# Optimization experiments

Hardware: AMD Instinct MI355X
Metric: run time of the kernel (lower is better)

## Reference

```python
import jax, jax.numpy as jnp
import numpy as np

V, E, DIN, DH = 8192, 4096, 512, 256
N_CLASSES = 2
EPS = 1e-5  # torch LayerNorm default
EDGE_P = 0.004  # ~33 nodes per hyperedge


def layernorm(x, g, b):
    m = jnp.mean(x, axis=-1, keepdims=True)
    v = jnp.mean((x - m) ** 2, axis=-1, keepdims=True)
    return (x - m) / jnp.sqrt(v + EPS) * g + b


def setup_inputs() -> dict:
    key = jax.random.key(0)
    ks = jax.random.split(key, 8)
    X = jax.random.normal(ks[0], (V, DIN), dtype=jnp.float32)
    # binary incidence matrix (|V|, |E|)
    H_inc = (jax.random.uniform(ks[1], (V, E)) < EDGE_P).astype(jnp.float32)
    Wp = jax.random.normal(ks[2], (DH, DIN), dtype=jnp.float32) * 0.02  # input_proj (no bias)
    W0 = jax.random.normal(ks[3], (DH, DH), dtype=jnp.float32) * 0.02
    W1 = jax.random.normal(ks[4], (DH, DH), dtype=jnp.float32) * 0.02
    g0 = jnp.ones((DH,), jnp.float32); b0 = jnp.zeros((DH,), jnp.float32)
    g1 = jnp.ones((DH,), jnp.float32); b1 = jnp.zeros((DH,), jnp.float32)
    Wc = jax.random.normal(ks[5], (N_CLASSES, DH), dtype=jnp.float32) * 0.02
    bc = jnp.zeros((N_CLASSES,), jnp.float32)
    return {"X": X, "H_inc": H_inc, "Wp": Wp, "W0": W0, "W1": W1,
            "g0": g0, "b0": b0, "g1": g1, "b1": b1, "Wc": Wc, "bc": bc}


def reference(X, H_inc, Wp, W0, W1, g0, b0, g1, b1, Wc, bc):
    # --- normalized incidence: H_tilde = D_v^{-1/2} H D_e^{-1/2}, 0 for isolated ---
    d_v = H_inc.sum(axis=1)   # (V,)
    d_e = H_inc.sum(axis=0)   # (E,)
    dvi = jnp.where(d_v > 0, jnp.where(d_v > 0, d_v, 1.0) ** -0.5, 0.0)
    dei = jnp.where(d_e > 0, jnp.where(d_e > 0, d_e, 1.0) ** -0.5, 0.0)
    H_tilde = dvi[:, None] * H_inc * dei[None, :]            # (V, E)
    HHt = H_tilde @ H_tilde.T                                # (V, V)

    # input projection
    Xh = X @ Wp.T                                            # (V, DH)

    # L=2 message-passing layers with residual + LayerNorm
    for W, g, b in ((W0, g0, b0), (W1, g1, b1)):
        Xn = jax.nn.relu((HHt @ Xh) @ W.T)
        Xh = layernorm(Xh + Xn, g, b)

    # mean pool per hyperedge (== Python loop over E in the original):
    # z_e = mean of member node embeddings; zeros for empty hyperedges
    cnt = jnp.where(d_e > 0, d_e, 1.0)[:, None]              # (E, 1)
    z_E = (H_inc.T @ Xh) / cnt                               # (E, DH)

    logits = z_E @ Wc.T + bc                                 # (E, 2)
    return jax.nn.softmax(logits, axis=1)
```

## Files before the change

kernel.cpp:

```cpp
#include <hip/hip_runtime.h>
#include <math.h>

#define NV 8192
#define NE 4096
#define DIN 512
#define DH 256
#define CAP_E 96
#define CAP_V 64
#define NPROJ (NV / 32)
#define NSCAN (NV / 2)

#define OFF_XH   0
#define OFF_UB   (OFF_XH + NV*DH)
#define OFF_YB   (OFF_UB + NV*DH/2)
#define OFF_NCNT (OFF_YB + NE*DH/2)
#define OFF_ECNT (OFF_NCNT + NV)
#define OFF_EL   (OFF_ECNT + NE*16)
#define OFF_NL   (OFF_EL + NE*CAP_E)
#define OFF_XHB  (OFF_NL + NV*CAP_V)
#define OFF_Q    (OFF_XHB + NV*DH/2)

using bf16x8 = __attribute__((ext_vector_type(8))) short;
using f32x4  = __attribute__((ext_vector_type(4))) float;
using f32x4v = __attribute__((ext_vector_type(4))) float;

__device__ inline unsigned short f2bf(float f) {
    union { float f; unsigned u; } v; v.f = f;
    unsigned r = v.u + 0x7FFF + ((v.u >> 16) & 1);
    return (unsigned short)(r >> 16);
}
__device__ inline float b2f(unsigned short s) {
    union { unsigned u; float f; } v; v.u = ((unsigned)s) << 16; return v.f;
}

__device__ inline void u_gemm_from_lds(const short* __restrict__ sm,
                                       const float* __restrict__ W,
                                       unsigned short* __restrict__ Ub,
                                       int bm, int tid) {
    const int w = tid >> 6, lane = tid & 63;
    const int r15 = lane & 15, k8 = (lane >> 4) << 3;
    const int swz = lane ^ ((lane >> 3) & 6);
    f32x4 acc[2][4];
#pragma unroll
    for (int mi = 0; mi < 2; ++mi)
#pragma unroll
        for (int ni = 0; ni < 4; ++ni) acc[mi][ni] = (f32x4){0.f, 0.f, 0.f, 0.f};
#pragma unroll
    for (int kc = 0; kc < 8; ++kc) {
        bf16x8 af[2], bfr[4];
        af[0] = *(const bf16x8*)&sm[(0 * 8 + kc) * 512 + swz * 8];
        af[1] = *(const bf16x8*)&sm[(1 * 8 + kc) * 512 + swz * 8];
#pragma unroll
        for (int ni = 0; ni < 4; ++ni) {
            const float* wr = W + (size_t)(w * 64 + ni * 16 + r15) * DH + kc * 32 + k8;
            float4 b0 = *(const float4*)wr;
            float4 b1 = *(const float4*)(wr + 4);
            bf16x8 bv;
            bv[0] = (short)f2bf(b0.x); bv[1] = (short)f2bf(b0.y);
            bv[2] = (short)f2bf(b0.z); bv[3] = (short)f2bf(b0.w);
            bv[4] = (short)f2bf(b1.x); bv[5] = (short)f2bf(b1.y);
            bv[6] = (short)f2bf(b1.z); bv[7] = (short)f2bf(b1.w);
            bfr[ni] = bv;
        }
#pragma unroll
        for (int mi = 0; mi < 2; ++mi)
#pragma unroll
            for (int ni = 0; ni < 4; ++ni)
                acc[mi][ni] = __builtin_amdgcn_mfma_f32_16x16x32_bf16(
                    af[mi], bfr[ni], acc[mi][ni], 0, 0, 0);
    }
    const int quad = lane >> 4, cl = lane & 15;
#pragma unroll
    for (int mi = 0; mi < 2; ++mi)
#pragma unroll
        for (int ni = 0; ni < 4; ++ni)
#pragma unroll
            for (int r = 0; r < 4; ++r)
                Ub[(size_t)(bm + mi * 16 + quad * 4 + r) * DH + w * 64 + ni * 16 + cl]
                    = f2bf(acc[mi][ni][r]);
}

__global__ __launch_bounds__(256) void scan_proj(const float* __restrict__ H,
                                                 const float* __restrict__ X,
                                                 const float* __restrict__ Wp,
                                                 const float* __restrict__ W0,
                                                 float* __restrict__ Xh,
                                                 unsigned short* __restrict__ Ub,
                                                 int* __restrict__ edge_cnt,
                                                 int* __restrict__ node_cnt,
                                                 int* __restrict__ edge_list,
                                                 int* __restrict__ node_list) {
    __shared__ short AsBs[1024 + 8192];
    const int tid = threadIdx.x;
    if (blockIdx.x >= NPROJ) {
        const int w = tid >> 6, lane = tid & 63;
        const int v    = (blockIdx.x - NPROJ) * 2 + (w >> 1);
        const int half = w & 1;
        const f32x4v* H4 = (const f32x4v*)(H + (size_t)v * NE) + half * 512;
        f32x4v h[8];
#pragma unroll
        for (int it = 0; it < 8; ++it)
            h[it] = __builtin_nontemporal_load(&H4[lane + 64 * it]);
        unsigned m = 0u;
#pragma unroll
        for (int it = 0; it < 8; ++it) {
#pragma unroll
            for (int c = 0; c < 4; ++c)
                m |= (h[it][c] != 0.0f ? 1u : 0u) << (it * 4 + c);
        }
        int n = __builtin_popcount(m);
        int pre = n;
#pragma unroll
        for (int o = 1; o < 64; o <<= 1) {
            int t = __shfl_up(pre, o, 64);
            if (lane >= o) pre += t;
        }
        int total = __shfl(pre, 63, 64);
        int local = pre - n;
        int base = 0;
        if (lane == 0 && total > 0) base = atomicAdd(&node_cnt[v], total);
        base = __shfl(base, 0, 64) + local;
        const int ebase = half * 2048 + 4 * lane;
        int e_arr[4] = {0, 0, 0, 0};
        {
            unsigned mm = m;
#pragma unroll
            for (int u = 0; u < 4; ++u) {
                if (mm) {
                    int j = __builtin_ctz(mm);
                    mm &= mm - 1;
                    e_arr[u] = ebase + 256 * (j >> 2) + (j & 3);
                }
            }
        }
        int s_arr[4];
#pragma unroll
        for (int u = 0; u < 4; ++u)
            s_arr[u] = (u < n) ? atomicAdd(&edge_cnt[e_arr[u] << 4], 1) : 0;
#pragma unroll
        for (int u = 0; u < 4; ++u) {
            if (u < n) {
                if (s_arr[u] < CAP_E) edge_list[e_arr[u] * CAP_E + s_arr[u]] = v;
                int idx = base + u;
                if (idx < CAP_V) node_list[v * CAP_V + idx] = e_arr[u];
            }
        }
        if (n > 4) {
            unsigned mm = m;
            mm &= mm - 1; mm &= mm - 1; mm &= mm - 1; mm &= mm - 1;
            int k = 4;
            while (mm) {
                int j = __builtin_ctz(mm); mm &= mm - 1;
                int ee = ebase + 256 * (j >> 2) + (j & 3);
                int gc = atomicAdd(&edge_cnt[ee << 4], 1);
                if (gc < CAP_E) edge_list[ee * CAP_E + gc] = v;
                int idx = base + k;
                if (idx < CAP_V) node_list[v * CAP_V + idx] = ee;
                ++k;
            }
        }
        return;
    }
    short* As = AsBs;
    short* Bs = AsBs + 1024;
    const int K = DIN;
    const int lane = tid & 63;
    const int w    = tid >> 6;
    const int bm   = blockIdx.x * 32;
    const int swz  = lane ^ ((lane >> 3) & 6);
    float4 ar, br[8];
    ar = *(const float4*)(X + (size_t)(bm + (tid >> 3)) * K + ((tid & 7) << 2));
#pragma unroll
    for (int it = 0; it < 8; ++it) {
        int i = tid + it * 256;
        br[it] = *(const float4*)(Wp + (size_t)(i >> 3) * K + ((i & 7) << 2));
    }
    f32x4 acc[2][4];
#pragma unroll
    for (int mi = 0; mi < 2; ++mi)
#pragma unroll
        for (int ni = 0; ni < 4; ++ni) acc[mi][ni] = (f32x4){0.f, 0.f, 0.f, 0.f};
    for (int k0 = 0; k0 < K; k0 += 32) {
        __syncthreads();
        {
            int row = tid >> 3, kk = (tid & 7) << 2;
            int quad = kk >> 3, j = kk & 7;
            int ln = (row & 15) + (quad << 4);
            int pp = ln ^ ((ln >> 3) & 6);
            ushort4 u = {f2bf(ar.x), f2bf(ar.y), f2bf(ar.z), f2bf(ar.w)};
            *(ushort4*)&As[(row >> 4) * 512 + pp * 8 + j] = u;
        }
#pragma unroll
        for (int it = 0; it < 8; ++it) {
            int i = tid + it * 256;
            int row = i >> 3, kk = (i & 7) << 2;
            int quad = kk >> 3, j = kk & 7;
            int ln = (row & 15) + (quad << 4);
            int pp = ln ^ ((ln >> 3) & 6);
            float4 v = br[it];
            ushort4 u = {f2bf(v.x), f2bf(v.y), f2bf(v.z), f2bf(v.w)};
            *(ushort4*)&Bs[(row >> 4) * 512 + pp * 8 + j] = u;
        }
        __syncthreads();
        if (k0 + 32 < K) {
            int kn = k0 + 32;
            ar = *(const float4*)(X + (size_t)(bm + (tid >> 3)) * K + kn + ((tid & 7) << 2));
#pragma unroll
            for (int it = 0; it < 8; ++it) {
                int i = tid + it * 256;
                br[it] = *(const float4*)(Wp + (size_t)(i >> 3) * K + kn + ((i & 7) << 2));
            }
        }
        bf16x8 af[2], bfr[4];
        af[0] = *(const bf16x8*)&As[0 * 512 + swz * 8];
        af[1] = *(const bf16x8*)&As[1 * 512 + swz * 8];
#pragma unroll
        for (int ni = 0; ni < 4; ++ni)
            bfr[ni] = *(const bf16x8*)&Bs[(w * 4 + ni) * 512 + swz * 8];
#pragma unroll
        for (int mi = 0; mi < 2; ++mi)
#pragma unroll
            for (int ni = 0; ni < 4; ++ni)
                acc[mi][ni] = __builtin_amdgcn_mfma_f32_16x16x32_bf16(
                    af[mi], bfr[ni], acc[mi][ni], 0, 0, 0);
    }
    const int quad = lane >> 4, cl = lane & 15;
    __syncthreads();
#pragma unroll
    for (int mi = 0; mi < 2; ++mi)
#pragma unroll
        for (int ni = 0; ni < 4; ++ni)
#pragma unroll
            for (int r = 0; r < 4; ++r) {
                float v = acc[mi][ni][r];
                int rl  = mi * 16 + quad * 4 + r;
                int col = w * 64 + ni * 16 + cl;
                Xh[(size_t)(bm + rl) * DH + col] = v;
                int kc = col >> 5, kk = col & 31;
                int q2 = kk >> 3, j = kk & 7;
                int ln = (rl & 15) + (q2 << 4);
                int pp = ln ^ ((ln >> 3) & 6);
                AsBs[(mi * 8 + kc) * 512 + pp * 8 + j] = (short)f2bf(v);
            }
    __syncthreads();
    u_gemm_from_lds(AsBs, W0, Ub, bm, tid);
}

__global__ __launch_bounds__(256) void gemm_u(const unsigned short* __restrict__ A,
                                              const float* __restrict__ W,
                                              unsigned short* __restrict__ U) {
    const int K = DH;
    __shared__ short As[2048];
    __shared__ short Bs[16384];
    const int tid  = threadIdx.x;
    const int lane = tid & 63;
    const int w    = tid >> 6;
    const int bm   = blockIdx.x * 32;
    const int swz  = lane ^ ((lane >> 3) & 6);

    uint4 ar; float4 br[16];
    ar = *(const uint4*)(A + (size_t)(bm + (tid >> 3)) * K + ((tid & 7) << 3));
#pragma unroll
    for (int it = 0; it < 16; ++it) {
        int i = tid + it * 256;
        br[it] = *(const float4*)(W + (size_t)(i >> 4) * K + ((i & 15) << 2));
    }
    f32x4 acc[2][4];
#pragma unroll
    for (int mi = 0; mi < 2; ++mi)
#pragma unroll
        for (int ni = 0; ni < 4; ++ni) acc[mi][ni] = (f32x4){0.f, 0.f, 0.f, 0.f};

    for (int k0 = 0; k0 < K; k0 += 64) {
        __syncthreads();
        {
            int row = tid >> 3, kq = tid & 7;
            int kc = kq >> 2, quad = kq & 3;
            int ln = (row & 15) + (quad << 4);
            int pp = ln ^ ((ln >> 3) & 6);
            *(uint4*)&As[((row >> 4) * 2 + kc) * 512 + pp * 8] = ar;
        }
#pragma unroll
        for (int it = 0; it < 16; ++it) {
            int i = tid + it * 256;
            int row = i >> 4, kk = (i & 15) << 2;
            int kc = kk >> 5, quad = (kk >> 3) & 3, j = kk & 7;
            int ln = (row & 15) + (quad << 4);
            int pp = ln ^ ((ln >> 3) & 6);
            float4 v = br[it];
            ushort4 u = {f2bf(v.x), f2bf(v.y), f2bf(v.z), f2bf(v.w)};
            *(ushort4*)&Bs[((row >> 4) * 2 + kc) * 512 + pp * 8 + j] = u;
        }
        __syncthreads();
        if (k0 + 64 < K) {
            int kn = k0 + 64;
            ar = *(const uint4*)(A + (size_t)(bm + (tid >> 3)) * K + kn + ((tid & 7) << 3));
#pragma unroll
            for (int it = 0; it < 16; ++it) {
                int i = tid + it * 256;
                br[it] = *(const float4*)(W + (size_t)(i >> 4) * K + kn + ((i & 15) << 2));
            }
        }
#pragma unroll
        for (int kc = 0; kc < 2; ++kc) {
            bf16x8 af[2], bfr[4];
            af[0] = *(const bf16x8*)&As[(0 * 2 + kc) * 512 + swz * 8];
            af[1] = *(const bf16x8*)&As[(1 * 2 + kc) * 512 + swz * 8];
#pragma unroll
            for (int ni = 0; ni < 4; ++ni)
                bfr[ni] = *(const bf16x8*)&Bs[((w * 4 + ni) * 2 + kc) * 512 + swz * 8];
#pragma unroll
            for (int mi = 0; mi < 2; ++mi)
#pragma unroll
                for (int ni = 0; ni < 4; ++ni)
                    acc[mi][ni] = __builtin_amdgcn_mfma_f32_16x16x32_bf16(
                        af[mi], bfr[ni], acc[mi][ni], 0, 0, 0);
        }
    }
    const int quad = lane >> 4, cl = lane & 15;
#pragma unroll
    for (int mi = 0; mi < 2; ++mi)
#pragma unroll
        for (int ni = 0; ni < 4; ++ni)
#pragma unroll
            for (int r = 0; r < 4; ++r)
                U[(size_t)(bm + mi * 16 + quad * 4 + r) * DH + w * 64 + ni * 16 + cl]
                    = f2bf(acc[mi][ni][r]);
}

__global__ __launch_bounds__(64) void edge_gather(const unsigned short* __restrict__ Ub,
                                                  const int* __restrict__ edge_cnt,
                                                  const int* __restrict__ edge_list,
                                                  const int* __restrict__ node_cnt,
                                                  unsigned short* __restrict__ Yb) {
    int e = blockIdx.x;
    int tid = threadIdx.x;
    __shared__ int   lv[CAP_E];
    __shared__ float lc[CAP_E];
    int tc = edge_cnt[e << 4];
    int cnt = min(tc, CAP_E);
    for (int j = tid; j < cnt; j += 64) {
        int v = edge_list[e * CAP_E + j];
        lv[j] = v * (DH / 4);
        lc[j] = rsqrtf((float)node_cnt[v]);
    }
    __syncthreads();
    const ushort4* X4 = (const ushort4*)Ub;
    float4 a[8];
#pragma unroll
    for (int u = 0; u < 8; ++u) a[u] = (float4){0.f, 0.f, 0.f, 0.f};
    int i = 0;
    for (; i + 8 <= cnt; i += 8) {
#pragma unroll
        for (int u = 0; u < 8; ++u) {
            ushort4 h = X4[lv[i + u] + tid]; float c = lc[i + u];
            a[u].x = fmaf(c, b2f(h.x), a[u].x); a[u].y = fmaf(c, b2f(h.y), a[u].y);
            a[u].z = fmaf(c, b2f(h.z), a[u].z); a[u].w = fmaf(c, b2f(h.w), a[u].w);
        }
    }
    for (; i < cnt; ++i) {
        ushort4 h = X4[lv[i] + tid]; float c = lc[i];
        a[0].x = fmaf(c, b2f(h.x), a[0].x); a[0].y = fmaf(c, b2f(h.y), a[0].y);
        a[0].z = fmaf(c, b2f(h.z), a[0].z); a[0].w = fmaf(c, b2f(h.w), a[0].w);
    }
#pragma unroll
    for (int u = 4; u > 0; u >>= 1)
#pragma unroll
        for (int q = 0; q < u; ++q) {
            a[q].x += a[q + u].x; a[q].y += a[q + u].y;
            a[q].z += a[q + u].z; a[q].w += a[q + u].w;
        }
    float de = tc > 0 ? rsqrtf((float)tc) : 0.f;
    ushort4 o = {f2bf(de * a[0].x), f2bf(de * a[0].y),
                 f2bf(de * a[0].z), f2bf(de * a[0].w)};
    ((ushort4*)Yb)[e * (DH / 4) + tid] = o;
}

__global__ __launch_bounds__(64) void node_ln(const unsigned short* __restrict__ Yb,
                                              const int* __restrict__ node_cnt,
                                              const int* __restrict__ node_list,
                                              const int* __restrict__ edge_cnt,
                                              float* __restrict__ Xh,
                                              unsigned short* __restrict__ Xhb,
                                              const float* __restrict__ g,
                                              const float* __restrict__ b) {
    int v = blockIdx.x;
    int tid = threadIdx.x;
    __shared__ int   le[CAP_V];
    __shared__ float lc[CAP_V];
    int tc = node_cnt[v];
    int cnt = min(tc, CAP_V);
    if (tid < cnt) {
        int e = node_list[v * CAP_V + tid];
        le[tid] = e * (DH / 4);
        lc[tid] = rsqrtf((float)edge_cnt[e << 4]);
    }
    __syncthreads();
    const ushort4* Y4 = (const ushort4*)Yb;
    float4 a[8];
#pragma unroll
    for (int u = 0; u < 8; ++u) a[u] = (float4){0.f, 0.f, 0.f, 0.f};
    int i = 0;
    for (; i + 8 <= cnt; i += 8) {
#pragma unroll
        for (int u = 0; u < 8; ++u) {
            ushort4 h = Y4[le[i + u] + tid]; float c = lc[i + u];
            a[u].x = fmaf(c, b2f(h.x), a[u].x); a[u].y = fmaf(c, b2f(h.y), a[u].y);
            a[u].z = fmaf(c, b2f(h.z), a[u].z); a[u].w = fmaf(c, b2f(h.w), a[u].w);
        }
    }
    for (; i < cnt; ++i) {
        ushort4 h = Y4[le[i] + tid]; float c = lc[i];
        a[0].x = fmaf(c, b2f(h.x), a[0].x); a[0].y = fmaf(c, b2f(h.y), a[0].y);
        a[0].z = fmaf(c, b2f(h.z), a[0].z); a[0].w = fmaf(c, b2f(h.w), a[0].w);
    }
#pragma unroll
    for (int u = 4; u > 0; u >>= 1)
#pragma unroll
        for (int q = 0; q < u; ++q) {
            a[q].x += a[q + u].x; a[q].y += a[q + u].y;
            a[q].z += a[q + u].z; a[q].w += a[q + u].w;
        }
    float dv = tc > 0 ? rsqrtf((float)tc) : 0.f;
    float4 xr = ((const float4*)Xh)[v * (DH / 4) + tid];
    float x0 = xr.x + fmaxf(dv * a[0].x, 0.f);
    float x1 = xr.y + fmaxf(dv * a[0].y, 0.f);
    float x2 = xr.z + fmaxf(dv * a[0].z, 0.f);
    float x3 = xr.w + fmaxf(dv * a[0].w, 0.f);
    float s = (x0 + x1) + (x2 + x3);
    float q = fmaf(x0, x0, fmaf(x1, x1, fmaf(x2, x2, x3 * x3)));
#pragma unroll
    for (int o = 1; o < 64; o <<= 1) {
        s += __shfl_xor(s, o, 64);
        q += __shfl_xor(q, o, 64);
    }
    float m = s * (1.0f / DH);
    float var = q * (1.0f / DH) - m * m;
    float rstd = rsqrtf(var + 1e-5f);
    float4 g4 = ((const float4*)g)[tid];
    float4 b4 = ((const float4*)b)[tid];
    float4 o;
    o.x = (x0 - m) * rstd * g4.x + b4.x;
    o.y = (x1 - m) * rstd * g4.y + b4.y;
    o.z = (x2 - m) * rstd * g4.z + b4.z;
    o.w = (x3 - m) * rstd * g4.w + b4.w;
    ((float4*)Xh)[v * (DH / 4) + tid] = o;
    ushort4 ob = {f2bf(o.x), f2bf(o.y), f2bf(o.z), f2bf(o.w)};
    ((ushort4*)Xhb)[v * (DH / 4) + tid] = ob;
}

__global__ __launch_bounds__(64) void node_ln_q(const unsigned short* __restrict__ Yb,
                                                const int* __restrict__ node_cnt,
                                                const int* __restrict__ node_list,
                                                const int* __restrict__ edge_cnt,
                                                const float* __restrict__ Xh,
                                                const float* __restrict__ g,
                                                const float* __restrict__ b,
                                                const float* __restrict__ Wc,
                                                float2* __restrict__ qout) {
    int v = blockIdx.x;
    int tid = threadIdx.x;
    __shared__ int   le[CAP_V];
    __shared__ float lc[CAP_V];
    int tc = node_cnt[v];
    int cnt = min(tc, CAP_V);
    if (tid < cnt) {
        int e = node_list[v * CAP_V + tid];
        le[tid] = e * (DH / 4);
        lc[tid] = rsqrtf((float)edge_cnt[e << 4]);
    }
    __syncthreads();
    const ushort4* Y4 = (const ushort4*)Yb;
    float4 a[8];
#pragma unroll
    for (int u = 0; u < 8; ++u) a[u] = (float4){0.f, 0.f, 0.f, 0.f};
    int i = 0;
    for (; i + 8 <= cnt; i += 8) {
#pragma unroll
        for (int u = 0; u < 8; ++u) {
            ushort4 h = Y4[le[i + u] + tid]; float c = lc[i + u];
            a[u].x = fmaf(c, b2f(h.x), a[u].x); a[u].y = fmaf(c, b2f(h.y), a[u].y);
            a[u].z = fmaf(c, b2f(h.z), a[u].z); a[u].w = fmaf(c, b2f(h.w), a[u].w);
        }
    }
    for (; i < cnt; ++i) {
        ushort4 h = Y4[le[i] + tid]; float c = lc[i];
        a[0].x = fmaf(c, b2f(h.x), a[0].x); a[0].y = fmaf(c, b2f(h.y), a[0].y);
        a[0].z = fmaf(c, b2f(h.z), a[0].z); a[0].w = fmaf(c, b2f(h.w), a[0].w);
    }
#pragma unroll
    for (int u = 4; u > 0; u >>= 1)
#pragma unroll
        for (int q = 0; q < u; ++q) {
            a[q].x += a[q + u].x; a[q].y += a[q + u].y;
            a[q].z += a[q + u].z; a[q].w += a[q + u].w;
        }
    float dv = tc > 0 ? rsqrtf((float)tc) : 0.f;
    float4 xr = ((const float4*)Xh)[v * (DH / 4) + tid];
    float x0 = xr.x + fmaxf(dv * a[0].x, 0.f);
    float x1 = xr.y + fmaxf(dv * a[0].y, 0.f);
    float x2 = xr.z + fmaxf(dv * a[0].z, 0.f);
    float x3 = xr.w + fmaxf(dv * a[0].w, 0.f);
    float s = (x0 + x1) + (x2 + x3);
    float q = fmaf(x0, x0, fmaf(x1, x1, fmaf(x2, x2, x3 * x3)));
#pragma unroll
    for (int o = 1; o < 64; o <<= 1) {
        s += __shfl_xor(s, o, 64);
        q += __shfl_xor(q, o, 64);
    }
    float m = s * (1.0f / DH);
    float var = q * (1.0f / DH) - m * m;
    float rstd = rsqrtf(var + 1e-5f);
    float4 g4 = ((const float4*)g)[tid];
    float4 b4 = ((const float4*)b)[tid];
    float o0 = b2f(f2bf((x0 - m) * rstd * g4.x + b4.x));
    float o1 = b2f(f2bf((x1 - m) * rstd * g4.y + b4.y));
    float o2 = b2f(f2bf((x2 - m) * rstd * g4.z + b4.z));
    float o3 = b2f(f2bf((x3 - m) * rstd * g4.w + b4.w));
    const float4* W4 = (const float4*)Wc;
    float4 w0 = W4[tid], w1 = W4[64 + tid];
    float p0 = o0 * w0.x + o1 * w0.y + o2 * w0.z + o3 * w0.w;
    float p1 = o0 * w1.x + o1 * w1.y + o2 * w1.z + o3 * w1.w;
#pragma unroll
    for (int off = 32; off > 0; off >>= 1) {
        p0 += __shfl_down(p0, off, 64);
        p1 += __shfl_down(p1, off, 64);
    }
    if (tid == 0) qout[v] = make_float2(p0, p1);
}

__global__ __launch_bounds__(256) void pool_q(const float2* __restrict__ q,
                                              const int* __restrict__ edge_cnt,
                                              const int* __restrict__ edge_list,
                                              const float* __restrict__ bc,
                                              float* __restrict__ out) {
    const int tid = threadIdx.x;
    const int w = tid >> 6, lane = tid & 63;
    const int e = blockIdx.x * 4 + w;
    int tc = edge_cnt[e << 4];
    int cnt = min(tc, CAP_E);
    float s0 = 0.f, s1 = 0.f;
    for (int j = lane; j < cnt; j += 64) {
        int v = edge_list[e * CAP_E + j];
        float2 qq = q[v];
        s0 += qq.x; s1 += qq.y;
    }
#pragma unroll
    for (int o = 32; o > 0; o >>= 1) {
        s0 += __shfl_down(s0, o, 64);
        s1 += __shfl_down(s1, o, 64);
    }
    if (lane == 0) {
        float inv = tc > 0 ? 1.0f / (float)tc : 1.0f;
        float l0 = s0 * inv + bc[0], l1 = s1 * inv + bc[1];
        float mx = fmaxf(l0, l1);
        float e0 = expf(l0 - mx), e1 = expf(l1 - mx);
        float sden = 1.0f / (e0 + e1);
        out[e * 2 + 0] = e0 * sden;
        out[e * 2 + 1] = e1 * sden;
    }
}

extern "C" void kernel_launch(void* const* d_in, const int* in_sizes, int n_in,
                              void* d_out, int out_size, void* d_ws, size_t ws_size,
                              hipStream_t stream) {
    const float* X  = (const float*)d_in[0];
    const float* H  = (const float*)d_in[1];
    const float* Wp = (const float*)d_in[2];
    const float* W0 = (const float*)d_in[3];
    const float* W1 = (const float*)d_in[4];
    const float* g0 = (const float*)d_in[5];
    const float* b0 = (const float*)d_in[6];
    const float* g1 = (const float*)d_in[7];
    const float* b1 = (const float*)d_in[8];
    const float* Wc = (const float*)d_in[9];
    const float* bc = (const float*)d_in[10];
    float* out = (float*)d_out;

    float* ws = (float*)d_ws;
    float* Xh  = ws + OFF_XH;
    unsigned short* Ub  = (unsigned short*)(ws + OFF_UB);
    unsigned short* Yb  = (unsigned short*)(ws + OFF_YB);
    int* node_cnt  = (int*)(ws + OFF_NCNT);
    int* edge_cnt  = (int*)(ws + OFF_ECNT);
    int* edge_list = (int*)(ws + OFF_EL);
    int* node_list = (int*)(ws + OFF_NL);
    unsigned short* Xhb = (unsigned short*)(ws + OFF_XHB);
    float2* qbuf = (float2*)(ws + OFF_Q);

    hipMemsetAsync(node_cnt, 0, (size_t)(NV + NE * 16) * sizeof(int), stream);

    scan_proj<<<NPROJ + NSCAN, 256, 0, stream>>>(H, X, Wp, W0, Xh, Ub,
                                                 edge_cnt, node_cnt, edge_list, node_list);

    edge_gather<<<NE, 64, 0, stream>>>(Ub, edge_cnt, edge_list, node_cnt, Yb);
    node_ln<<<NV, 64, 0, stream>>>(Yb, node_cnt, node_list, edge_cnt,
                                   Xh, Xhb, g0, b0);
    gemm_u<<<NV / 32, 256, 0, stream>>>(Xhb, W1, Ub);
    edge_gather<<<NE, 64, 0, stream>>>(Ub, edge_cnt, edge_list, node_cnt, Yb);
    node_ln_q<<<NV, 64, 0, stream>>>(Yb, node_cnt, node_list, edge_cnt,
                                     Xh, g1, b1, Wc, qbuf);

    pool_q<<<NE / 4, 256, 0, stream>>>(qbuf, edge_cnt, edge_list, bc, out);
}
```

Measured before the change: 281.2 us.

## Split incidence scan into bitmask compression and separate list-building kernel

The fused scan kernel now only reads the dense incidence matrix and writes a per-node 4096-bit mask using wave ballots. A new build_lists kernel reads these masks, prefix-sums the counts, and fills the edge and node adjacency lists with atomics. This takes the atomic scatter work out of the bandwidth-bound streaming pass so the 128 MB read can run at full rate. The cost is an extra kernel launch and a small bitmask buffer in the workspace.

```diff
diff --git a/kernel.cpp b/kernel.cpp
--- a/kernel.cpp
+++ b/kernel.cpp
@@ -8,7 +8,7 @@
 #define CAP_E 96
 #define CAP_V 64
 #define NPROJ (NV / 32)
-#define NSCAN (NV / 2)
+#define NCOMP (NV / 2)
 
 #define OFF_XH   0
 #define OFF_UB   (OFF_XH + NV*DH)
@@ -19,10 +19,12 @@
 #define OFF_NL   (OFF_EL + NE*CAP_E)
 #define OFF_XHB  (OFF_NL + NV*CAP_V)
 #define OFF_Q    (OFF_XHB + NV*DH/2)
+#define OFF_BITS (OFF_Q + NV*2)
 
 using bf16x8 = __attribute__((ext_vector_type(8))) short;
 using f32x4  = __attribute__((ext_vector_type(4))) float;
 using f32x4v = __attribute__((ext_vector_type(4))) float;
+typedef unsigned long long u64;
 
 __device__ inline unsigned short f2bf(float f) {
     union { float f; unsigned u; } v; v.f = f;
@@ -80,84 +82,38 @@
                     = f2bf(acc[mi][ni][r]);
 }
 
-__global__ __launch_bounds__(256) void scan_proj(const float* __restrict__ H,
-                                                 const float* __restrict__ X,
-                                                 const float* __restrict__ Wp,
-                                                 const float* __restrict__ W0,
-                                                 float* __restrict__ Xh,
-                                                 unsigned short* __restrict__ Ub,
-                                                 int* __restrict__ edge_cnt,
-                                                 int* __restrict__ node_cnt,
-                                                 int* __restrict__ edge_list,
-                                                 int* __restrict__ node_list) {
+__global__ __launch_bounds__(256) void compress_proj(const float* __restrict__ H,
+                                                     const float* __restrict__ X,
+                                                     const float* __restrict__ Wp,
+                                                     const float* __restrict__ W0,
+                                                     float* __restrict__ Xh,
+                                                     unsigned short* __restrict__ Ub,
+                                                     u64* __restrict__ bits) {
     __shared__ short AsBs[1024 + 8192];
     const int tid = threadIdx.x;
     if (blockIdx.x >= NPROJ) {
         const int w = tid >> 6, lane = tid & 63;
-        const int v    = (blockIdx.x - NPROJ) * 2 + (w >> 1);
-        const int half = w & 1;
-        const f32x4v* H4 = (const f32x4v*)(H + (size_t)v * NE) + half * 512;
-        f32x4v h[8];
-#pragma unroll
-        for (int it = 0; it < 8; ++it)
-            h[it] = __builtin_nontemporal_load(&H4[lane + 64 * it]);
-        unsigned m = 0u;
-#pragma unroll
-        for (int it = 0; it < 8; ++it) {
-#pragma unroll
-            for (int c = 0; c < 4; ++c)
-                m |= (h[it][c] != 0.0f ? 1u : 0u) << (it * 4 + c);
-        }
-        int n = __builtin_popcount(m);
-        int pre = n;
-#pragma unroll
-        for (int o = 1; o < 64; o <<= 1) {
-            int t = __shfl_up(pre, o, 64);
-            if (lane >= o) pre += t;
-        }
-        int total = __shfl(pre, 63, 64);
-        int local = pre - n;
-        int base = 0;
-        if (lane == 0 && total > 0) base = atomicAdd(&node_cnt[v], total);
-        base = __shfl(base, 0, 64) + local;
-        const int ebase = half * 2048 + 4 * lane;
-        int e_arr[4] = {0, 0, 0, 0};
-        {
-            unsigned mm = m;
-#pragma unroll
-            for (int u = 0; u < 4; ++u) {
-                if (mm) {
-                    int j = __builtin_ctz(mm);
-                    mm &= mm - 1;
-                    e_arr[u] = ebase + 256 * (j >> 2) + (j & 3);
+        const int vb = (blockIdx.x - NPROJ) * 2;
+        const f32x4v* H4 = (const f32x4v*)(H + (size_t)vb * NE);
+        f32x4v h[2][4];
+#pragma unroll
+        for (int r = 0; r < 2; ++r)
+#pragma unroll
+            for (int it = 0; it < 4; ++it)
+                h[r][it] = __builtin_nontemporal_load(&H4[r * 1024 + tid + it * 256]);
+        u64 myword[2] = {0ULL, 0ULL};
+#pragma unroll
+        for (int r = 0; r < 2; ++r)
+#pragma unroll
+            for (int it = 0; it < 4; ++it)
+#pragma unroll
+                for (int c = 0; c < 4; ++c) {
+                    u64 b = __ballot(h[r][it][c] != 0.0f);
+                    if (lane == it * 4 + c) myword[r] = b;
                 }
-            }
-        }
-        int s_arr[4];
-#pragma unroll
-        for (int u = 0; u < 4; ++u)
-            s_arr[u] = (u < n) ? atomicAdd(&edge_cnt[e_arr[u] << 4], 1) : 0;
-#pragma unroll
-        for (int u = 0; u < 4; ++u) {
-            if (u < n) {
-                if (s_arr[u] < CAP_E) edge_list[e_arr[u] * CAP_E + s_arr[u]] = v;
-                int idx = base + u;
-                if (idx < CAP_V) node_list[v * CAP_V + idx] = e_arr[u];
-            }
-        }
-        if (n > 4) {
-            unsigned mm = m;
-            mm &= mm - 1; mm &= mm - 1; mm &= mm - 1; mm &= mm - 1;
-            int k = 4;
-            while (mm) {
-                int j = __builtin_ctz(mm); mm &= mm - 1;
-                int ee = ebase + 256 * (j >> 2) + (j & 3);
-                int gc = atomicAdd(&edge_cnt[ee << 4], 1);
-                if (gc < CAP_E) edge_list[ee * CAP_E + gc] = v;
-                int idx = base + k;
-                if (idx < CAP_V) node_list[v * CAP_V + idx] = ee;
-                ++k;
-            }
+        if (lane < 16) {
+            bits[(size_t)vb * 64 + w * 16 + lane]       = myword[0];
+            bits[(size_t)(vb + 1) * 64 + w * 16 + lane] = myword[1];
         }
         return;
     }
@@ -244,6 +200,39 @@
             }
     __syncthreads();
     u_gemm_from_lds(AsBs, W0, Ub, bm, tid);
+}
+
+__global__ __launch_bounds__(256) void build_lists(const u64* __restrict__ bits,
+                                                   int* __restrict__ edge_cnt,
+                                                   int* __restrict__ node_cnt,
+                                                   int* __restrict__ edge_list,
+                                                   int* __restrict__ node_list) {
+    const int tid = threadIdx.x;
+    const int w = tid >> 6, lane = tid & 63;
+    const int v = blockIdx.x * 4 + w;
+    u64 m = bits[(size_t)v * 64 + lane];
+    int n = __builtin_popcountll(m);
+    int pre = n;
+#pragma unroll
+    for (int o = 1; o < 64; o <<= 1) {
+        int t = __shfl_up(pre, o, 64);
+        if (lane >= o) pre += t;
+    }
+    int total = __shfl(pre, 63, 64);
+    if (lane == 0) node_cnt[v] = total;
+    int base = pre - n;
+    const int w2 = lane >> 4, r = lane & 15, it = r >> 2, c = r & 3;
+    const int cbase = 4 * (w2 * 64 + it * 256) + c;
+    int k = 0;
+    while (m) {
+        int l = __builtin_ctzll(m); m &= m - 1;
+        int e = cbase + 4 * l;
+        int gc = atomicAdd(&edge_cnt[e << 4], 1);
+        if (gc < CAP_E) edge_list[e * CAP_E + gc] = v;
+        int idx = base + k;
+        if (idx < CAP_V) node_list[v * CAP_V + idx] = e;
+        ++k;
+    }
 }
 
 __global__ __launch_bounds__(256) void gemm_u(const unsigned short* __restrict__ A,
@@ -587,11 +576,13 @@
     int* node_list = (int*)(ws + OFF_NL);
     unsigned short* Xhb = (unsigned short*)(ws + OFF_XHB);
     float2* qbuf = (float2*)(ws + OFF_Q);
+    u64* bits = (u64*)(ws + OFF_BITS);
 
     hipMemsetAsync(node_cnt, 0, (size_t)(NV + NE * 16) * sizeof(int), stream);
 
-    scan_proj<<<NPROJ + NSCAN, 256, 0, stream>>>(H, X, Wp, W0, Xh, Ub,
-                                                 edge_cnt, node_cnt, edge_list, node_list);
+    compress_proj<<<NPROJ + NCOMP, 256, 0, stream>>>(H, X, Wp, W0, Xh, Ub, bits);
+    build_lists<<<NV / 4, 256, 0, stream>>>(bits, edge_cnt, node_cnt,
+                                            edge_list, node_list);
 
     edge_gather<<<NE, 64, 0, stream>>>(Ub, edge_cnt, edge_list, node_cnt, Yb);
     node_ln<<<NV, 64, 0, stream>>>(Yb, node_cnt, node_list, edge_cnt,
```

Measured after the change: 285.2 us. Within noise of the previous version (+1.4%).
